# Kernel optimization log

Hardware: AMD Instinct MI355X
Metric: run time of the kernel (lower is better)

The kernel has to match this reference:

```python
import jax, jax.numpy as jnp
import numpy as np
import math

E = 512
W = 16


def overlap_and_add(signal, frame_step):
    """signal: [..., frames, frame_length] -> [..., frame_step*(frames-1)+frame_length]."""
    outer = signal.shape[:-2]
    frames, frame_length = signal.shape[-2:]
    subframe_length = math.gcd(frame_length, frame_step)
    subframe_step = frame_step // subframe_length
    subframes_per_frame = frame_length // subframe_length
    output_size = frame_step * (frames - 1) + frame_length
    output_subframes = output_size // subframe_length

    # [B, frames*subframes_per_frame, subframe_length]
    B = int(np.prod(outer)) if outer else 1
    sub = signal.reshape(B, frames * subframes_per_frame, subframe_length)
    # destination subframe index for each source subframe
    idx = (jnp.arange(frames)[:, None] * subframe_step
           + jnp.arange(subframes_per_frame)[None, :]).reshape(-1)
    out = jnp.zeros((B, output_subframes, subframe_length), signal.dtype)
    out = out.at[:, idx, :].add(sub)
    return out.reshape(*outer, output_size)


def setup_inputs() -> dict:
    key = jax.random.key(0)
    k1, k2 = jax.random.split(key)
    mixture_w = jax.random.normal(k1, (8, 2, 16000, E), dtype=jnp.float32)
    # nn.Linear(E, W).weight has shape [W, E]
    basis_weight = jax.random.normal(k2, (W, E), dtype=jnp.float32) * (1.0 / math.sqrt(E))
    return {"mixture_w": mixture_w, "basis_weight": basis_weight}


def reference(mixture_w, basis_weight):
    # est_source: [..., frames, W]
    est_source = jnp.einsum('bckE,wE->bckw', mixture_w, basis_weight)
    return overlap_and_add(est_source, W // 2)
```

## Files before the change

kernel.cpp:

```cpp
#include <hip/hip_runtime.h>


#define FRAMES 16000
#define EDIM   512
#define OUTF   16001
#define OUT_PER_BC 128008
#define BATCHES 16
#define OFPW    128

__global__ __launch_bounds__(128, 2)
void decoder_kernel(const float* __restrict__ A,
                    const float* __restrict__ B,
                    float* __restrict__ out)
{
    const int t   = threadIdx.x;
    const int wid = t >> 6;
    const int l   = t & 63;
    const int wq  = l & 7;
    const int ksl = l >> 3;
    const int bc  = blockIdx.y;
    const int o0  = (blockIdx.x * 2 + wid) * OFPW;

    __shared__ float ring[2][16][16];

    const float4* B4 = (const float4*)B;
    float4 Bw[2][2][8];
    #pragma unroll
    for (int w = 0; w < 2; ++w)
        #pragma unroll
        for (int h = 0; h < 2; ++h)
            #pragma unroll
            for (int j = 0; j < 8; ++j)
                Bw[w][h][j] = B4[(2*wq + w) * 128 + ksl*16 + h*8 + j];

    const float4* Abc = (const float4*)(A + (size_t)bc * FRAMES * EDIM);

    float4 Abuf[2][8];

    auto loadHalf = [&](float4* dst, int f, int h) {
        int fc = f; if (fc < 0) fc = 0; if (fc >= FRAMES) fc = FRAMES - 1;
        const float4* p = Abc + (size_t)fc * 128 + ksl*16 + h*8;
        #pragma unroll
        for (int j = 0; j < 8; ++j) dst[j] = p[j];
    };

    auto processFrame = [&](int f) {
        loadHalf(Abuf[1], f, 1);
        float acc[2][2] = {{0.f,0.f},{0.f,0.f}};
        #pragma unroll
        for (int j = 0; j < 8; ++j) {
            const float4 a = Abuf[0][j];
            acc[0][0] = fmaf(a.x, Bw[0][0][j].x, acc[0][0]);
            acc[0][0] = fmaf(a.y, Bw[0][0][j].y, acc[0][0]);
            acc[0][0] = fmaf(a.z, Bw[0][0][j].z, acc[0][0]);
            acc[0][0] = fmaf(a.w, Bw[0][0][j].w, acc[0][0]);
            acc[1][0] = fmaf(a.x, Bw[1][0][j].x, acc[1][0]);
            acc[1][0] = fmaf(a.y, Bw[1][0][j].y, acc[1][0]);
            acc[1][0] = fmaf(a.z, Bw[1][0][j].z, acc[1][0]);
            acc[1][0] = fmaf(a.w, Bw[1][0][j].w, acc[1][0]);
        }
        loadHalf(Abuf[0], f + 1, 0);
        #pragma unroll
        for (int j = 0; j < 8; ++j) {
            const float4 a = Abuf[1][j];
            acc[0][1] = fmaf(a.x, Bw[0][1][j].x, acc[0][1]);
            acc[0][1] = fmaf(a.y, Bw[0][1][j].y, acc[0][1]);
            acc[0][1] = fmaf(a.z, Bw[0][1][j].z, acc[0][1]);
            acc[0][1] = fmaf(a.w, Bw[0][1][j].w, acc[0][1]);
            acc[1][1] = fmaf(a.x, Bw[1][1][j].x, acc[1][1]);
            acc[1][1] = fmaf(a.y, Bw[1][1][j].y, acc[1][1]);
            acc[1][1] = fmaf(a.z, Bw[1][1][j].z, acc[1][1]);
            acc[1][1] = fmaf(a.w, Bw[1][1][j].w, acc[1][1]);
        }
        float r0 = acc[0][0] + acc[0][1];
        float r1 = acc[1][0] + acc[1][1];
        r0 += __shfl_xor(r0, 8);   r1 += __shfl_xor(r1, 8);
        r0 += __shfl_xor(r0, 16);  r1 += __shfl_xor(r1, 16);
        r0 += __shfl_xor(r0, 32);  r1 += __shfl_xor(r1, 32);
        if (f < 0 || f >= FRAMES) { r0 = 0.f; r1 = 0.f; }
        if (ksl == 0) {
            *(float2*)&ring[wid][f & 15][2*wq] = make_float2(r0, r1);
        }
    };

    loadHalf(Abuf[0], o0 - 1, 0);
    processFrame(o0 - 1);

    for (int b = 0; b < BATCHES; ++b) {
        const int cf = o0 + b * 8;
        #pragma unroll
        for (int r = 0; r < 8; ++r) processFrame(cf + r);
        __syncthreads();
        const int fr = cf + (l >> 3);
        const float v = ring[wid][fr & 15][l & 7]
                      + ring[wid][(fr - 1) & 15][8 + (l & 7)];
        if (fr < OUTF)
            out[(size_t)bc * OUT_PER_BC + (size_t)cf * 8 + l] = v;
    }
}

extern "C" void kernel_launch(void* const* d_in, const int* in_sizes, int n_in,
                              void* d_out, int out_size, void* d_ws, size_t ws_size,
                              hipStream_t stream) {
    const float* A   = (const float*)d_in[0];
    const float* B   = (const float*)d_in[1];
    float*       out = (float*)d_out;

    dim3 grid(63, 16, 1);
    decoder_kernel<<<grid, dim3(128, 1, 1), 0, stream>>>(A, B, out);
}
```

Baseline: 749.1 us.

## Stage A frames through swizzled LDS with coalesced loads and single-wave blocks

Each frame's 512 floats are now loaded by the whole wave as two contiguous float4 rows, written into a double-buffered, XOR-swizzled LDS slot, and read back per k-slice. Before, each lane read a strided 16-float4 chunk straight from global. Blocks shrink to one wave and the grid doubles, and the next frame is prefetched two frames ahead. The aim is better global load coalescing and more latency hiding, at the cost of an LDS round trip and a barrier per frame.

```diff
diff --git a/kernel.cpp b/kernel.cpp
--- a/kernel.cpp
+++ b/kernel.cpp
@@ -2,101 +2,106 @@
 
 
 #define FRAMES 16000
-#define EDIM   512
-#define OUTF   16001
 #define OUT_PER_BC 128008
-#define BATCHES 16
-#define OFPW    128
+#define OFPW 128
 
-__global__ __launch_bounds__(128, 2)
+__global__ __launch_bounds__(64, 2)
 void decoder_kernel(const float* __restrict__ A,
                     const float* __restrict__ B,
                     float* __restrict__ out)
 {
-    const int t   = threadIdx.x;
-    const int wid = t >> 6;
-    const int l   = t & 63;
+    __shared__ float4 Aslot[2][128];
+    __shared__ float  ring[16][16];
+
+    const int l   = threadIdx.x;
     const int wq  = l & 7;
     const int ksl = l >> 3;
     const int bc  = blockIdx.y;
-    const int o0  = (blockIdx.x * 2 + wid) * OFPW;
-
-    __shared__ float ring[2][16][16];
+    const int o0  = blockIdx.x * OFPW;
 
     const float4* B4 = (const float4*)B;
-    float4 Bw[2][2][8];
+    float4 Bw0[16], Bw1[16];
     #pragma unroll
-    for (int w = 0; w < 2; ++w)
+    for (int j = 0; j < 16; ++j) {
+        Bw0[j] = B4[(2*wq    ) * 128 + ksl*16 + j];
+        Bw1[j] = B4[(2*wq + 1) * 128 + ksl*16 + j];
+    }
+
+    const float4* Abc = (const float4*)A + (size_t)bc * FRAMES * 128;
+
+    const int p0 = l ^ (l >> 4);
+    const int p1 = 64 + (l ^ ((4 + (l >> 4)) & 7));
+
+    float4 V[2][2];
+
+    auto ldA = [&](int par, int f) {
+        int fc = f < 0 ? 0 : (f >= FRAMES ? FRAMES - 1 : f);
+        const float4* p = Abc + (size_t)fc * 128;
+        V[par][0] = p[l];
+        V[par][1] = p[64 + l];
+    };
+    auto stA = [&](int par) {
+        Aslot[par][p0] = V[par][0];
+        Aslot[par][p1] = V[par][1];
+    };
+    auto epilogue = [&](int fb) {
+        const int fr = fb + (l >> 3);
+        const float v = ring[fr & 15][l & 7] + ring[(fr - 1) & 15][8 + (l & 7)];
+        if (fr <= FRAMES)
+            out[(size_t)bc * OUT_PER_BC + (size_t)fb * 8 + l] = v;
+    };
+    auto compute = [&](int f, int s) {
+        float a00 = 0.f, a01 = 0.f, a10 = 0.f, a11 = 0.f;
         #pragma unroll
-        for (int h = 0; h < 2; ++h)
-            #pragma unroll
-            for (int j = 0; j < 8; ++j)
-                Bw[w][h][j] = B4[(2*wq + w) * 128 + ksl*16 + h*8 + j];
-
-    const float4* Abc = (const float4*)(A + (size_t)bc * FRAMES * EDIM);
-
-    float4 Abuf[2][8];
-
-    auto loadHalf = [&](float4* dst, int f, int h) {
-        int fc = f; if (fc < 0) fc = 0; if (fc >= FRAMES) fc = FRAMES - 1;
-        const float4* p = Abc + (size_t)fc * 128 + ksl*16 + h*8;
-        #pragma unroll
-        for (int j = 0; j < 8; ++j) dst[j] = p[j];
-    };
-
-    auto processFrame = [&](int f) {
-        loadHalf(Abuf[1], f, 1);
-        float acc[2][2] = {{0.f,0.f},{0.f,0.f}};
-        #pragma unroll
-        for (int j = 0; j < 8; ++j) {
-            const float4 a = Abuf[0][j];
-            acc[0][0] = fmaf(a.x, Bw[0][0][j].x, acc[0][0]);
-            acc[0][0] = fmaf(a.y, Bw[0][0][j].y, acc[0][0]);
-            acc[0][0] = fmaf(a.z, Bw[0][0][j].z, acc[0][0]);
-            acc[0][0] = fmaf(a.w, Bw[0][0][j].w, acc[0][0]);
-            acc[1][0] = fmaf(a.x, Bw[1][0][j].x, acc[1][0]);
-            acc[1][0] = fmaf(a.y, Bw[1][0][j].y, acc[1][0]);
-            acc[1][0] = fmaf(a.z, Bw[1][0][j].z, acc[1][0]);
-            acc[1][0] = fmaf(a.w, Bw[1][0][j].w, acc[1][0]);
+        for (int j = 0; j < 16; ++j) {
+            const float4 a  = Aslot[s][ksl*16 + (j ^ ksl)];
+            const float4 b0 = Bw0[j];
+            const float4 b1 = Bw1[j];
+            if (j & 1) {
+                a01 = fmaf(a.x, b0.x, a01); a01 = fmaf(a.y, b0.y, a01);
+                a01 = fmaf(a.z, b0.z, a01); a01 = fmaf(a.w, b0.w, a01);
+                a11 = fmaf(a.x, b1.x, a11); a11 = fmaf(a.y, b1.y, a11);
+                a11 = fmaf(a.z, b1.z, a11); a11 = fmaf(a.w, b1.w, a11);
+            } else {
+                a00 = fmaf(a.x, b0.x, a00); a00 = fmaf(a.y, b0.y, a00);
+                a00 = fmaf(a.z, b0.z, a00); a00 = fmaf(a.w, b0.w, a00);
+                a10 = fmaf(a.x, b1.x, a10); a10 = fmaf(a.y, b1.y, a10);
+                a10 = fmaf(a.z, b1.z, a10); a10 = fmaf(a.w, b1.w, a10);
+            }
         }
-        loadHalf(Abuf[0], f + 1, 0);
-        #pragma unroll
-        for (int j = 0; j < 8; ++j) {
-            const float4 a = Abuf[1][j];
-            acc[0][1] = fmaf(a.x, Bw[0][1][j].x, acc[0][1]);
-            acc[0][1] = fmaf(a.y, Bw[0][1][j].y, acc[0][1]);
-            acc[0][1] = fmaf(a.z, Bw[0][1][j].z, acc[0][1]);
-            acc[0][1] = fmaf(a.w, Bw[0][1][j].w, acc[0][1]);
-            acc[1][1] = fmaf(a.x, Bw[1][1][j].x, acc[1][1]);
-            acc[1][1] = fmaf(a.y, Bw[1][1][j].y, acc[1][1]);
-            acc[1][1] = fmaf(a.z, Bw[1][1][j].z, acc[1][1]);
-            acc[1][1] = fmaf(a.w, Bw[1][1][j].w, acc[1][1]);
-        }
-        float r0 = acc[0][0] + acc[0][1];
-        float r1 = acc[1][0] + acc[1][1];
+        float r0 = a00 + a01;
+        float r1 = a10 + a11;
         r0 += __shfl_xor(r0, 8);   r1 += __shfl_xor(r1, 8);
         r0 += __shfl_xor(r0, 16);  r1 += __shfl_xor(r1, 16);
         r0 += __shfl_xor(r0, 32);  r1 += __shfl_xor(r1, 32);
         if (f < 0 || f >= FRAMES) { r0 = 0.f; r1 = 0.f; }
         if (ksl == 0) {
-            *(float2*)&ring[wid][f & 15][2*wq] = make_float2(r0, r1);
+            ring[f & 15][2*wq    ] = r0;
+            ring[f & 15][2*wq + 1] = r1;
         }
     };
 
-    loadHalf(Abuf[0], o0 - 1, 0);
-    processFrame(o0 - 1);
+    ldA(1, o0 - 1);
+    ldA(0, o0);
+    stA(1);
+    __syncthreads();
+    ldA(1, o0 + 1);
+    compute(o0 - 1, 1);
 
-    for (int b = 0; b < BATCHES; ++b) {
-        const int cf = o0 + b * 8;
+    for (int b = 0; b < 16; ++b) {
         #pragma unroll
-        for (int r = 0; r < 8; ++r) processFrame(cf + r);
-        __syncthreads();
-        const int fr = cf + (l >> 3);
-        const float v = ring[wid][fr & 15][l & 7]
-                      + ring[wid][(fr - 1) & 15][8 + (l & 7)];
-        if (fr < OUTF)
-            out[(size_t)bc * OUT_PER_BC + (size_t)cf * 8 + l] = v;
+        for (int r = 0; r < 8; ++r) {
+            const int f   = o0 + b * 8 + r;
+            const int par = r & 1;
+            stA(par);
+            __syncthreads();
+            if (r == 0 && b > 0) epilogue(f - 8);
+            ldA(par, f + 2);
+            compute(f, par);
+        }
     }
+    __syncthreads();
+    epilogue(o0 + 120);
 }
 
 extern "C" void kernel_launch(void* const* d_in, const int* in_sizes, int n_in,
@@ -106,6 +111,6 @@
     const float* B   = (const float*)d_in[1];
     float*       out = (float*)d_out;
 
-    dim3 grid(63, 16, 1);
-    decoder_kernel<<<grid, dim3(128, 1, 1), 0, stream>>>(A, B, out);
+    dim3 grid(126, 16, 1);
+    decoder_kernel<<<grid, dim3(64, 1, 1), 0, stream>>>(A, B, out);
 }
```

After: 753.2 us. No clear change (+0.5%).
